# Kernel tuning notes

Hardware: AMD Instinct MI355X
Metric: run time of the kernel (lower is better)

## Reference

```python
import jax, jax.numpy as jnp
import numpy as np

NUM_ITERATIONS = 3


def squash(t, axis=-1):
    # scale * t / ||t|| with scale = ||t||^2 / (1 + ||t||^2)
    sq = jnp.sum(t * t, axis=axis, keepdims=True)
    scale = sq / (1.0 + sq)
    return scale * t / jnp.sqrt(sq)


def setup_inputs() -> dict:
    key = jax.random.key(0)
    k1, k2 = jax.random.split(key)
    B, N, Ci = 256, 1152, 8   # batch, num_route_nodes, in_channels
    C, Co = 10, 16            # num_capsules, out_channels
    x = jax.random.normal(k1, (B, N, Ci), dtype=jnp.float32)
    route_weights = jax.random.normal(k2, (C, N, Ci, Co), dtype=jnp.float32)
    return {"x": x, "route_weights": route_weights}


def reference(x, route_weights):
    # priors: [C, B, N, 1, Co] (matches x[None,:,:,None,:] @ W[:,None])
    priors = jnp.einsum('bni,cnio->cbno', x, route_weights)[:, :, :, None, :]
    logits = jnp.zeros_like(priors)
    outputs = None
    for i in range(NUM_ITERATIONS):
        probs = jax.nn.softmax(logits, axis=2)  # softmax over route nodes (dim=2)
        outputs = squash(jnp.sum(probs * priors, axis=2, keepdims=True))  # [C,B,1,1,Co]
        if i != NUM_ITERATIONS - 1:
            # agreement: [C,B,N,1,1], broadcasts into logits
            logits = logits + jnp.sum(priors * outputs, axis=-1, keepdims=True)
    return outputs
```

## Files before the change

kernel.cpp:

```cpp
#include <hip/hip_runtime.h>
#include <hip/hip_fp16.h>

#define NB    384
#define ROWS  3
#define N_ROUTE 1152
#define C_IN  8
#define C_OUT 16

template<int CTRL>
__device__ __forceinline__ float dpp_add(float v) {
    int t = __builtin_amdgcn_update_dpp(0, __float_as_int(v), CTRL, 0xF, 0xF, true);
    return v + __int_as_float(t);
}
__device__ __forceinline__ float wave_sum63(float v) {
    v = dpp_add<0x111>(v);
    v = dpp_add<0x112>(v);
    v = dpp_add<0x114>(v);
    v = dpp_add<0x118>(v);
    v = dpp_add<0x142>(v);
    v = dpp_add<0x143>(v);
    return v;
}

__global__ __launch_bounds__(NB, 2)
void capsule_routing(const float* __restrict__ x,
                     const float* __restrict__ W,
                     float* __restrict__ out)
{
    __shared__ unsigned int P[N_ROUTE * 8];
    __shared__ float red[6][20];
    __shared__ float vfin[16];

    const int t    = threadIdx.x;
    const int bid  = blockIdx.x;
    const int c    = bid >> 8;
    const int b    = bid & 255;
    const int lane = t & 63;
    const int wid  = t >> 6;

    {
        const int og = t & 3;
        const int nl = t >> 2;
        const float* __restrict__ xb = x + (size_t)b * (N_ROUTE * C_IN);
        const float* __restrict__ Wc = W + (size_t)c * (N_ROUTE * C_IN * C_OUT);
        #pragma unroll 2
        for (int pp = 0; pp < 12; ++pp) {
            const int n = pp * 96 + nl;
            const float4 x0 = *reinterpret_cast<const float4*>(xb + n * C_IN);
            const float4 x1 = *reinterpret_cast<const float4*>(xb + n * C_IN + 4);
            const float xs[8] = {x0.x, x0.y, x0.z, x0.w, x1.x, x1.y, x1.z, x1.w};
            const float* __restrict__ wp = Wc + (size_t)n * (C_IN * C_OUT) + (og << 2);
            float4 acc = make_float4(0.f, 0.f, 0.f, 0.f);
            #pragma unroll
            for (int i = 0; i < 8; ++i) {
                const float4 w = *reinterpret_cast<const float4*>(wp + i * C_OUT);
                acc.x = fmaf(xs[i], w.x, acc.x);
                acc.y = fmaf(xs[i], w.y, acc.y);
                acc.z = fmaf(xs[i], w.z, acc.z);
                acc.w = fmaf(xs[i], w.w, acc.w);
            }
            const int s    = (n >> 2) & 7;
            const int base = n << 3;
            __half2 h0 = __floats2half2_rn(acc.x, acc.y);
            __half2 h1 = __floats2half2_rn(acc.z, acc.w);
            P[base + (((og << 1)    ) ^ s)] = *reinterpret_cast<unsigned int*>(&h0);
            P[base + (((og << 1) + 1) ^ s)] = *reinterpret_cast<unsigned int*>(&h1);
        }
    }
    __syncthreads();

    float vprev[16];
    #pragma unroll
    for (int o = 0; o < 16; ++o) vprev[o] = 0.f;
    float lg[ROWS] = {0.f, 0.f, 0.f};

    #pragma unroll
    for (int it = 0; it < 3; ++it) {
        float sp[16];
        #pragma unroll
        for (int o = 0; o < 16; ++o) sp[o] = 0.f;
        float zp = (it == 0) ? (float)ROWS : 0.f;

        #pragma unroll
        for (int k = 0; k < ROWS; ++k) {
            const int n = t + k * NB;
            const int s = (n >> 2) & 7;
            const unsigned int* __restrict__ pr = &P[n << 3];
            __half2 h[8];
            #pragma unroll
            for (int j = 0; j < 8; ++j) {
                const unsigned int w = pr[j ^ s];
                h[j] = *reinterpret_cast<const __half2*>(&w);
            }
            float e;
            if (it == 0) {
                e = 1.f;
            } else {
                float d = 0.f;
                #pragma unroll
                for (int j = 0; j < 8; ++j) {
                    d = fmaf(__low2float(h[j]),  vprev[2 * j],     d);
                    d = fmaf(__high2float(h[j]), vprev[2 * j + 1], d);
                }
                lg[k] += d;
                e = __expf(lg[k]);
                zp += e;
            }
            #pragma unroll
            for (int j = 0; j < 8; ++j) {
                sp[2 * j]     = fmaf(e, __low2float(h[j]),  sp[2 * j]);
                sp[2 * j + 1] = fmaf(e, __high2float(h[j]), sp[2 * j + 1]);
            }
        }

        #pragma unroll
        for (int o = 0; o < 16; ++o) sp[o] = wave_sum63(sp[o]);
        zp = wave_sum63(zp);
        if (lane == 63) {
            #pragma unroll
            for (int o = 0; o < 16; ++o) red[wid][o] = sp[o];
            red[wid][16] = zp;
        }
        __syncthreads();

        if (t < 16) {
            float tot = 0.f, Zt = 0.f;
            #pragma unroll
            for (int w2 = 0; w2 < 6; ++w2) {
                tot += red[w2][t];
                Zt  += red[w2][16];
            }
            const float so = tot / Zt;
            float sq = so * so;
            #pragma unroll
            for (int off = 8; off >= 1; off >>= 1) sq += __shfl_xor(sq, off);
            const float fac = sqrtf(sq) / (1.f + sq);
            const float vo  = so * fac;
            if (it == 2) out[((size_t)bid << 4) + t] = vo;
            else         vfin[t] = vo;
        }
        if (it < 2) {
            __syncthreads();
            const float4 v0 = *reinterpret_cast<const float4*>(&vfin[0]);
            const float4 v1 = *reinterpret_cast<const float4*>(&vfin[4]);
            const float4 v2 = *reinterpret_cast<const float4*>(&vfin[8]);
            const float4 v3 = *reinterpret_cast<const float4*>(&vfin[12]);
            vprev[0]=v0.x;  vprev[1]=v0.y;  vprev[2]=v0.z;  vprev[3]=v0.w;
            vprev[4]=v1.x;  vprev[5]=v1.y;  vprev[6]=v1.z;  vprev[7]=v1.w;
            vprev[8]=v2.x;  vprev[9]=v2.y;  vprev[10]=v2.z; vprev[11]=v2.w;
            vprev[12]=v3.x; vprev[13]=v3.y; vprev[14]=v3.z; vprev[15]=v3.w;
        }
    }
}

extern "C" void kernel_launch(void* const* d_in, const int* in_sizes, int n_in,
                              void* d_out, int out_size, void* d_ws, size_t ws_size,
                              hipStream_t stream)
{
    const float* x   = (const float*)d_in[0];
    const float* W   = (const float*)d_in[1];
    float*       out = (float*)d_out;
    capsule_routing<<<dim3(10 * 256), dim3(NB), 0, stream>>>(x, W, out);
}
```

Baseline: 137.6 us.

## Pre-convert weights to fp16 lane-major layout and keep priors in registers

A new pre-pass kernel converts W to fp16 pairs in a coalesced, lane-interleaved chunk layout stored in the workspace. The main kernel then computes priors with packed fp16 dot products (fdot2) straight into registers, which removes the LDS prior buffer and its bank swizzle. The agreement dot product also uses fdot2 against an fp16-packed output vector. This halves weight bytes read and drops the LDS footprint, at the cost of an extra launch each call and more rounding from fp16 accumulation of inputs. The old LDS path is kept as a fallback when the workspace is too small.

```diff
diff --git a/kernel.cpp b/kernel.cpp
--- a/kernel.cpp
+++ b/kernel.cpp
@@ -1,11 +1,34 @@
 #include <hip/hip_runtime.h>
 #include <hip/hip_fp16.h>
 
-#define NB    384
-#define ROWS  3
+#define NB     384
+#define ROWS   3
 #define N_ROUTE 1152
-#define C_IN  8
-#define C_OUT 16
+#define RB     18
+#define NCHUNK 16
+
+typedef __fp16 half2v __attribute__((ext_vector_type(2)));
+
+__device__ __forceinline__ float fdot2u(unsigned int a, unsigned int b, float c) {
+#if __has_builtin(__builtin_amdgcn_fdot2)
+    half2v ha, hb;
+    __builtin_memcpy(&ha, &a, 4);
+    __builtin_memcpy(&hb, &b, 4);
+    return __builtin_amdgcn_fdot2(ha, hb, c, false);
+#else
+    const __half2 h_a = *reinterpret_cast<const __half2*>(&a);
+    const __half2 h_b = *reinterpret_cast<const __half2*>(&b);
+    return fmaf(__low2float(h_a), __low2float(h_b),
+           fmaf(__high2float(h_a), __high2float(h_b), c));
+#endif
+}
+
+__device__ __forceinline__ unsigned int pkh(float a, float b) {
+    half2v h = __builtin_amdgcn_cvt_pkrtz(a, b);
+    unsigned int u;
+    __builtin_memcpy(&u, &h, 4);
+    return u;
+}
 
 template<int CTRL>
 __device__ __forceinline__ float dpp_add(float v) {
@@ -22,12 +45,39 @@
     return v;
 }
 
+__global__ __launch_bounds__(256, 2)
+void convert_w(const float* __restrict__ W, uint4* __restrict__ Wh)
+{
+    const int tid = blockIdx.x * 256 + threadIdx.x;
+    const int c = tid / N_ROUTE;
+    const int n = tid - c * N_ROUTE;
+    const float* __restrict__ src = W + (size_t)tid * 128;
+    unsigned int ch[16][4];
+    #pragma unroll
+    for (int ip = 0; ip < 4; ++ip) {
+        float a[16], bb[16];
+        #pragma unroll
+        for (int q = 0; q < 4; ++q) {
+            const float4 va = *reinterpret_cast<const float4*>(src + (2*ip)   * 16 + q*4);
+            const float4 vb = *reinterpret_cast<const float4*>(src + (2*ip+1) * 16 + q*4);
+            a[q*4+0]=va.x;  a[q*4+1]=va.y;  a[q*4+2]=va.z;  a[q*4+3]=va.w;
+            bb[q*4+0]=vb.x; bb[q*4+1]=vb.y; bb[q*4+2]=vb.z; bb[q*4+3]=vb.w;
+        }
+        #pragma unroll
+        for (int o = 0; o < 16; ++o) ch[o][ip] = pkh(a[o], bb[o]);
+    }
+    const int r = n >> 6, l = n & 63;
+    uint4* __restrict__ dst = Wh + ((size_t)(c * RB + r) * NCHUNK) * 64 + l;
+    #pragma unroll
+    for (int o = 0; o < 16; ++o)
+        dst[o * 64] = make_uint4(ch[o][0], ch[o][1], ch[o][2], ch[o][3]);
+}
+
 __global__ __launch_bounds__(NB, 2)
-void capsule_routing(const float* __restrict__ x,
-                     const float* __restrict__ W,
-                     float* __restrict__ out)
+void capsule_routing_reg(const float* __restrict__ x,
+                         const uint4* __restrict__ Wh,
+                         float* __restrict__ out)
 {
-    __shared__ unsigned int P[N_ROUTE * 8];
     __shared__ float red[6][20];
     __shared__ float vfin[16];
 
@@ -38,22 +88,139 @@
     const int lane = t & 63;
     const int wid  = t >> 6;
 
+    unsigned int p2[ROWS][8];
+    {
+        const float* __restrict__ xb = x + (size_t)b * (N_ROUTE * 8);
+        const uint4* __restrict__ Wc = Wh + (size_t)c * RB * NCHUNK * 64;
+        #pragma unroll
+        for (int k = 0; k < ROWS; ++k) {
+            const int r = wid + 6 * k;
+            const int n = (r << 6) + lane;
+            const float4 x0 = *reinterpret_cast<const float4*>(xb + n * 8);
+            const float4 x1 = *reinterpret_cast<const float4*>(xb + n * 8 + 4);
+            const unsigned int xh[4] = { pkh(x0.x, x0.y), pkh(x0.z, x0.w),
+                                         pkh(x1.x, x1.y), pkh(x1.z, x1.w) };
+            const uint4* __restrict__ wr = Wc + (size_t)r * NCHUNK * 64 + lane;
+            #pragma unroll
+            for (int j = 0; j < 8; ++j) {
+                const uint4 w0 = wr[(2 * j)     * 64];
+                const uint4 w1 = wr[(2 * j + 1) * 64];
+                float d0 = fdot2u(xh[0], w0.x, 0.f);
+                d0 = fdot2u(xh[1], w0.y, d0);
+                d0 = fdot2u(xh[2], w0.z, d0);
+                d0 = fdot2u(xh[3], w0.w, d0);
+                float d1 = fdot2u(xh[0], w1.x, 0.f);
+                d1 = fdot2u(xh[1], w1.y, d1);
+                d1 = fdot2u(xh[2], w1.z, d1);
+                d1 = fdot2u(xh[3], w1.w, d1);
+                p2[k][j] = pkh(d0, d1);
+            }
+        }
+    }
+
+    float lg[ROWS] = {0.f, 0.f, 0.f};
+    unsigned int vph[8] = {0, 0, 0, 0, 0, 0, 0, 0};
+
+    #pragma unroll
+    for (int it = 0; it < 3; ++it) {
+        float sp[16];
+        #pragma unroll
+        for (int o = 0; o < 16; ++o) sp[o] = 0.f;
+        float zp = (it == 0) ? (float)ROWS : 0.f;
+
+        #pragma unroll
+        for (int k = 0; k < ROWS; ++k) {
+            float e;
+            if (it == 0) {
+                e = 1.f;
+            } else {
+                float d = 0.f;
+                #pragma unroll
+                for (int j = 0; j < 8; ++j) d = fdot2u(p2[k][j], vph[j], d);
+                lg[k] += d;
+                e = __expf(lg[k]);
+                zp += e;
+            }
+            #pragma unroll
+            for (int j = 0; j < 8; ++j) {
+                const __half2 h = *reinterpret_cast<const __half2*>(&p2[k][j]);
+                sp[2 * j]     = fmaf(e, __low2float(h),  sp[2 * j]);
+                sp[2 * j + 1] = fmaf(e, __high2float(h), sp[2 * j + 1]);
+            }
+        }
+
+        #pragma unroll
+        for (int o = 0; o < 16; ++o) sp[o] = wave_sum63(sp[o]);
+        zp = wave_sum63(zp);
+        if (lane == 63) {
+            #pragma unroll
+            for (int o = 0; o < 16; ++o) red[wid][o] = sp[o];
+            red[wid][16] = zp;
+        }
+        __syncthreads();
+
+        if (t < 16) {
+            float tot = 0.f, Zt = 0.f;
+            #pragma unroll
+            for (int w2 = 0; w2 < 6; ++w2) {
+                tot += red[w2][t];
+                Zt  += red[w2][16];
+            }
+            const float so = tot / Zt;
+            float sq = so * so;
+            #pragma unroll
+            for (int off = 8; off >= 1; off >>= 1) sq += __shfl_xor(sq, off);
+            const float fac = sqrtf(sq) / (1.f + sq);
+            const float vo  = so * fac;
+            if (it == 2) out[((size_t)bid << 4) + t] = vo;
+            else         vfin[t] = vo;
+        }
+        if (it < 2) {
+            __syncthreads();
+            const float4 v0 = *reinterpret_cast<const float4*>(&vfin[0]);
+            const float4 v1 = *reinterpret_cast<const float4*>(&vfin[4]);
+            const float4 v2 = *reinterpret_cast<const float4*>(&vfin[8]);
+            const float4 v3 = *reinterpret_cast<const float4*>(&vfin[12]);
+            vph[0] = pkh(v0.x, v0.y);  vph[1] = pkh(v0.z, v0.w);
+            vph[2] = pkh(v1.x, v1.y);  vph[3] = pkh(v1.z, v1.w);
+            vph[4] = pkh(v2.x, v2.y);  vph[5] = pkh(v2.z, v2.w);
+            vph[6] = pkh(v3.x, v3.y);  vph[7] = pkh(v3.z, v3.w);
+        }
+    }
+}
+
+__global__ __launch_bounds__(NB, 2)
+void capsule_routing_lds(const float* __restrict__ x,
+                         const float* __restrict__ W,
+                         float* __restrict__ out)
+{
+    __shared__ unsigned int P[N_ROUTE * 8];
+    __shared__ float red[6][20];
+    __shared__ float vfin[16];
+
+    const int t    = threadIdx.x;
+    const int bid  = blockIdx.x;
+    const int c    = bid >> 8;
+    const int b    = bid & 255;
+    const int lane = t & 63;
+    const int wid  = t >> 6;
+
     {
         const int og = t & 3;
         const int nl = t >> 2;
-        const float* __restrict__ xb = x + (size_t)b * (N_ROUTE * C_IN);
-        const float* __restrict__ Wc = W + (size_t)c * (N_ROUTE * C_IN * C_OUT);
+        const float* __restrict__ xb = x + (size_t)b * (N_ROUTE * 8);
+        const float* __restrict__ Wc = W + (size_t)c * (N_ROUTE * 128);
         #pragma unroll 2
         for (int pp = 0; pp < 12; ++pp) {
             const int n = pp * 96 + nl;
-            const float4 x0 = *reinterpret_cast<const float4*>(xb + n * C_IN);
-            const float4 x1 = *reinterpret_cast<const float4*>(xb + n * C_IN + 4);
+            const float4 x0 = *reinterpret_cast<const float4*>(xb + n * 8);
+            const float4 x1 = *reinterpret_cast<const float4*>(xb + n * 8 + 4);
             const float xs[8] = {x0.x, x0.y, x0.z, x0.w, x1.x, x1.y, x1.z, x1.w};
-            const float* __restrict__ wp = Wc + (size_t)n * (C_IN * C_OUT) + (og << 2);
+            const float* __restrict__ wp = Wc + (size_t)n * 128 + (og << 2);
             float4 acc = make_float4(0.f, 0.f, 0.f, 0.f);
             #pragma unroll
             for (int i = 0; i < 8; ++i) {
-                const float4 w = *reinterpret_cast<const float4*>(wp + i * C_OUT);
+                const float4 w = *reinterpret_cast<const float4*>(wp + i * 16);
                 acc.x = fmaf(xs[i], w.x, acc.x);
                 acc.y = fmaf(xs[i], w.y, acc.y);
                 acc.z = fmaf(xs[i], w.z, acc.z);
@@ -61,10 +228,8 @@
             }
             const int s    = (n >> 2) & 7;
             const int base = n << 3;
-            __half2 h0 = __floats2half2_rn(acc.x, acc.y);
-            __half2 h1 = __floats2half2_rn(acc.z, acc.w);
-            P[base + (((og << 1)    ) ^ s)] = *reinterpret_cast<unsigned int*>(&h0);
-            P[base + (((og << 1) + 1) ^ s)] = *reinterpret_cast<unsigned int*>(&h1);
+            P[base + (((og << 1)    ) ^ s)] = pkh(acc.x, acc.y);
+            P[base + (((og << 1) + 1) ^ s)] = pkh(acc.z, acc.w);
         }
     }
     __syncthreads();
@@ -126,10 +291,7 @@
         if (t < 16) {
             float tot = 0.f, Zt = 0.f;
             #pragma unroll
-            for (int w2 = 0; w2 < 6; ++w2) {
-                tot += red[w2][t];
-                Zt  += red[w2][16];
-            }
+            for (int w2 = 0; w2 < 6; ++w2) { tot += red[w2][t]; Zt += red[w2][16]; }
             const float so = tot / Zt;
             float sq = so * so;
             #pragma unroll
@@ -141,14 +303,8 @@
         }
         if (it < 2) {
             __syncthreads();
-            const float4 v0 = *reinterpret_cast<const float4*>(&vfin[0]);
-            const float4 v1 = *reinterpret_cast<const float4*>(&vfin[4]);
-            const float4 v2 = *reinterpret_cast<const float4*>(&vfin[8]);
-            const float4 v3 = *reinterpret_cast<const float4*>(&vfin[12]);
-            vprev[0]=v0.x;  vprev[1]=v0.y;  vprev[2]=v0.z;  vprev[3]=v0.w;
-            vprev[4]=v1.x;  vprev[5]=v1.y;  vprev[6]=v1.z;  vprev[7]=v1.w;
-            vprev[8]=v2.x;  vprev[9]=v2.y;  vprev[10]=v2.z; vprev[11]=v2.w;
-            vprev[12]=v3.x; vprev[13]=v3.y; vprev[14]=v3.z; vprev[15]=v3.w;
+            #pragma unroll
+            for (int o = 0; o < 16; ++o) vprev[o] = vfin[o];
         }
     }
 }
@@ -160,5 +316,13 @@
     const float* x   = (const float*)d_in[0];
     const float* W   = (const float*)d_in[1];
     float*       out = (float*)d_out;
-    capsule_routing<<<dim3(10 * 256), dim3(NB), 0, stream>>>(x, W, out);
-}
+    const size_t WH_BYTES = (size_t)10 * RB * NCHUNK * 64 * sizeof(uint4);
+
+    if (ws_size >= WH_BYTES) {
+        uint4* Wh = (uint4*)d_ws;
+        convert_w<<<dim3(45), dim3(256), 0, stream>>>(W, Wh);
+        capsule_routing_reg<<<dim3(10 * 256), dim3(NB), 0, stream>>>(x, Wh, out);
+    } else {
+        capsule_routing_lds<<<dim3(10 * 256), dim3(NB), 0, stream>>>(x, W, out);
+    }
+}
```

Result: faster. 120.5 us (-12.4%).
